# Kernel optimization log

Hardware: AMD Instinct MI355X
Metric: run time of the kernel (lower is better)

Reference implementation:

```python
import jax, jax.numpy as jnp
import numpy as np

N = 100000
E = 1600000
NIN = 128
NOUT = 128


def setup_inputs() -> dict:
    key = jax.random.key(0)
    k1, k2, k3, k4 = jax.random.split(key, 4)
    x = jax.random.normal(k1, (N, NIN), dtype=jnp.float32)
    edge_index = jax.random.randint(k2, (2, E), 0, N, dtype=jnp.int64)
    edge_attr = jnp.ones((E,), dtype=jnp.float32)  # unused by GCNConv
    # PyG Linear weight is [out, in]; glorot-ish init
    W = jax.random.normal(k3, (NOUT, NIN), dtype=jnp.float32) / np.sqrt(NIN)
    b = jnp.zeros((NOUT,), dtype=jnp.float32)
    return {"x": x, "edge_index": edge_index, "edge_attr": edge_attr, "W": W, "b": b}


def reference(x, edge_index, edge_attr, W, b):
    # PyG GCNConv: add self-loops, symmetric degree normalization,
    # linear transform, scatter-add aggregation at destination, + bias.
    n = x.shape[0]
    loops = jnp.arange(n, dtype=edge_index.dtype)
    src = jnp.concatenate([edge_index[0], loops])  # [E+N]
    dst = jnp.concatenate([edge_index[1], loops])  # [E+N]
    # degree over destination (col) including self-loops, edge weight = 1
    deg = jax.ops.segment_sum(jnp.ones_like(dst, dtype=x.dtype), dst, num_segments=n)
    dinv = jnp.where(deg > 0, jax.lax.rsqrt(deg), 0.0)
    norm = dinv[src] * dinv[dst]  # [E+N]
    h = x @ W.T  # [N, NOUT]
    msg = h[src] * norm[:, None]  # [E+N, NOUT]
    out = jax.ops.segment_sum(msg, dst, num_segments=n)  # [N, NOUT]
    return out + b
```

## Files before the change

### kernel.cpp

```cpp
#include <hip/hip_runtime.h>

#define TPB 256
#define NBLK 256
#define BSH 8

typedef __attribute__((ext_vector_type(4))) float f32x4;
typedef __attribute__((ext_vector_type(8))) short short8;

__device__ __forceinline__ unsigned short f2bf(float f) {
    unsigned u = __float_as_uint(f);
    u = (u + 0x7fffu + ((u >> 16) & 1u)) >> 16;
    return (unsigned short)u;
}
__device__ __forceinline__ float bflo(unsigned u) { return __uint_as_float(u << 16); }
__device__ __forceinline__ float bfhi(unsigned u) { return __uint_as_float(u & 0xffff0000u); }


__global__ __launch_bounds__(256) void k_bhist(const int* __restrict__ dst,
                                               int* __restrict__ btotal, int E, int NB) {
    __shared__ int sh[512];
    for (int i = threadIdx.x; i < NB; i += 256) sh[i] = 0;
    __syncthreads();
    int chunk = (E + NBLK - 1) / NBLK;
    int lo = blockIdx.x * chunk;
    int hi = min(E, lo + chunk);
    for (int e = lo + threadIdx.x; e < hi; e += 256)
        atomicAdd(&sh[dst[e] >> BSH], 1);
    __syncthreads();
    for (int i = threadIdx.x; i < NB; i += 256)
        if (sh[i]) atomicAdd(&btotal[i], sh[i]);
}


__global__ __launch_bounds__(512) void k_bscan(const int* __restrict__ btotal,
                                               int* __restrict__ bbase, int* __restrict__ bcur,
                                               int* __restrict__ offsets, int E, int NB, int N) {
    __shared__ int tmp[2][512];
    int t = threadIdx.x;
    int v = (t < NB) ? btotal[t] : 0;
    tmp[0][t] = v;
    __syncthreads();
    int sb = 0;
    for (int d = 1; d < 512; d <<= 1) {
        int val = tmp[sb][t];
        if (t >= d) val += tmp[sb][t - d];
        tmp[sb ^ 1][t] = val;
        sb ^= 1;
        __syncthreads();
    }
    int excl = tmp[sb][t] - v;
    if (t < NB) { bbase[t] = excl; bcur[t] = excl; }
    if (t == 0) { bbase[NB] = E; offsets[N] = E; }
}


__global__ __launch_bounds__(256) void k_bscatter(const int* __restrict__ src,
                                                  const int* __restrict__ dst,
                                                  int* __restrict__ bcur,
                                                  int2* __restrict__ pairs, int E, int NB) {
    __shared__ int sh[512];
    __shared__ int sbase[512];
    for (int i = threadIdx.x; i < NB; i += 256) sh[i] = 0;
    __syncthreads();
    int chunk = (E + NBLK - 1) / NBLK;
    int lo = blockIdx.x * chunk;
    int hi = min(E, lo + chunk);
    for (int e = lo + threadIdx.x; e < hi; e += 256)
        atomicAdd(&sh[dst[e] >> BSH], 1);
    __syncthreads();
    for (int i = threadIdx.x; i < NB; i += 256) {
        int c = sh[i];
        sbase[i] = c ? atomicAdd(&bcur[i], c) : 0;
    }
    __syncthreads();
    for (int i = threadIdx.x; i < NB; i += 256) sh[i] = sbase[i];
    __syncthreads();
    for (int e = lo + threadIdx.x; e < hi; e += 256) {
        int d = dst[e];
        int pos = atomicAdd(&sh[d >> BSH], 1);
        pairs[pos] = make_int2(d, src[e]);
    }
}


__global__ __launch_bounds__(256) void k_bcsr(const int2* __restrict__ pairs,
                                              const int* __restrict__ bbase,
                                              int* __restrict__ offsets,
                                              int* __restrict__ sorted_src,
                                              float* __restrict__ dinv, int N) {
    __shared__ int hist[256];
    __shared__ int tmp[2][256];
    __shared__ int scur[256];
    int b = blockIdx.x;
    int s0 = bbase[b], s1 = bbase[b + 1];
    int t = threadIdx.x;
    hist[t] = 0;
    __syncthreads();
    for (int e = s0 + t; e < s1; e += 256)
        atomicAdd(&hist[pairs[e].x & 255], 1);
    __syncthreads();
    int v = hist[t];
    tmp[0][t] = v;
    __syncthreads();
    int sb = 0;
    for (int d = 1; d < 256; d <<= 1) {
        int val = tmp[sb][t];
        if (t >= d) val += tmp[sb][t - d];
        tmp[sb ^ 1][t] = val;
        sb ^= 1;
        __syncthreads();
    }
    int gbase = s0 + (tmp[sb][t] - v);
    scur[t] = gbase;
    int d = (b << BSH) + t;
    if (d < N) { offsets[d] = gbase; dinv[d] = rsqrtf((float)v + 1.0f); }
    __syncthreads();
    for (int e = s0 + t; e < s1; e += 256) {
        int2 pr = pairs[e];
        int pos = atomicAdd(&scur[pr.x & 255], 1);
        sorted_src[pos] = pr.y;
    }
}


__global__ void k_castW(const float* __restrict__ W, unsigned short* __restrict__ Wt) {
    int i = blockIdx.x * TPB + threadIdx.x;
    if (i < 128 * 128) Wt[i] = f2bf(W[i]);
}


__global__ __launch_bounds__(256) void k_gemm(const float* __restrict__ x,
                                              const unsigned short* __restrict__ Wt,
                                              const float* __restrict__ dinv,
                                              unsigned short* __restrict__ g, int n) {
    __shared__ unsigned short wb[128][136];
    const int tid = threadIdx.x;

    for (int chunk = tid; chunk < 2048; chunk += 256) {
        int nrow = chunk >> 4, k8 = (chunk & 15) << 3;
        *(uint4*)&wb[nrow][k8] = ((const uint4*)Wt)[chunk];
    }
    __syncthreads();

    const int lane = tid & 63;
    const int wid  = tid >> 6;
    const int l15  = lane & 15;
    const int quad = lane >> 4;
    const int row  = blockIdx.x * 64 + wid * 16 + l15;
    const int rowc = (row < n) ? row : (n - 1);

    f32x4 acc[8];
    #pragma unroll
    for (int t = 0; t < 8; ++t) acc[t] = (f32x4){0.f, 0.f, 0.f, 0.f};

    #pragma unroll
    for (int ks = 0; ks < 4; ++ks) {
        const int kb = ks * 32 + quad * 8;
        float4 a0 = *(const float4*)(x + (long)rowc * 128 + kb);
        float4 a1 = *(const float4*)(x + (long)rowc * 128 + kb + 4);
        union { unsigned short u[8]; short8 v; } af;
        af.u[0] = f2bf(a0.x); af.u[1] = f2bf(a0.y); af.u[2] = f2bf(a0.z); af.u[3] = f2bf(a0.w);
        af.u[4] = f2bf(a1.x); af.u[5] = f2bf(a1.y); af.u[6] = f2bf(a1.z); af.u[7] = f2bf(a1.w);
        #pragma unroll
        for (int t = 0; t < 8; ++t) {
            short8 bf = *(const short8*)&wb[t * 16 + l15][kb];
            acc[t] = __builtin_amdgcn_mfma_f32_16x16x32_bf16(af.v, bf, acc[t], 0, 0, 0);
        }
    }

    int   orow[4];
    float dv[4];
    #pragma unroll
    for (int r = 0; r < 4; ++r) {
        orow[r] = blockIdx.x * 64 + wid * 16 + quad * 4 + r;
        dv[r]   = (orow[r] < n) ? dinv[orow[r]] : 0.f;
    }
    #pragma unroll
    for (int t = 0; t < 8; ++t) {
        int col = t * 16 + l15;
        #pragma unroll
        for (int r = 0; r < 4; ++r) {
            if (orow[r] < n)
                g[(long)orow[r] * 128 + col] = f2bf(acc[t][r] * dv[r]);
        }
    }
}


__global__ __launch_bounds__(256) void k_aggregate(const int* __restrict__ sorted_src,
                                                   const int* __restrict__ offsets,
                                                   const unsigned short* __restrict__ g,
                                                   const float* __restrict__ dinv,
                                                   const float* __restrict__ b,
                                                   float* __restrict__ out, int n) {
    int d = blockIdx.x * (TPB / 32) + (threadIdx.x >> 5);
    if (d >= n) return;
    int c = (threadIdx.x & 31) << 2;

    int s0 = offsets[d];
    int s1 = offsets[d + 1];

    float4 acc = make_float4(0.f, 0.f, 0.f, 0.f);
    auto addrow = [&](int r) {
        uint2 p = *(const uint2*)(g + (long)r * 128 + c);
        acc.x += bflo(p.x); acc.y += bfhi(p.x);
        acc.z += bflo(p.y); acc.w += bfhi(p.y);
    };

    addrow(d);
    int e = s0;
    for (; e + 8 <= s1; e += 8) {
        int a[8];
        #pragma unroll
        for (int j = 0; j < 8; ++j) a[j] = sorted_src[e + j];
        #pragma unroll
        for (int j = 0; j < 8; ++j) addrow(a[j]);
    }
    for (; e + 4 <= s1; e += 4) {
        int a[4];
        #pragma unroll
        for (int j = 0; j < 4; ++j) a[j] = sorted_src[e + j];
        #pragma unroll
        for (int j = 0; j < 4; ++j) addrow(a[j]);
    }
    for (; e < s1; ++e) addrow(sorted_src[e]);

    float s = dinv[d];
    float4 bb = *(const float4*)(b + c);
    float4 r = make_float4(acc.x * s + bb.x, acc.y * s + bb.y,
                           acc.z * s + bb.z, acc.w * s + bb.w);
    *(float4*)(out + (long)d * 128 + c) = r;
}


extern "C" void kernel_launch(void* const* d_in, const int* in_sizes, int n_in,
                              void* d_out, int out_size, void* d_ws, size_t ws_size,
                              hipStream_t stream) {
    const float* x  = (const float*)d_in[0];
    const int*   ei = (const int*)d_in[1];
    const float* W  = (const float*)d_in[3];
    const float* b  = (const float*)d_in[4];
    float* out = (float*)d_out;

    const int N = in_sizes[0] / 128;
    const int E = in_sizes[1] / 2;
    const int* src = ei;
    const int* dst = ei + E;
    const int NB = (N + 255) >> BSH;

    char* p = (char*)d_ws;
    auto carve = [&](size_t bytes) { char* q = p; p += (bytes + 255) & ~(size_t)255; return q; };
    int*            btotal     = (int*)           carve(512 * 4);
    int*            bbase      = (int*)           carve(513 * 4);
    int*            bcur       = (int*)           carve(512 * 4);
    int*            offsets    = (int*)           carve((size_t)(N + 1) * 4);
    float*          dinv       = (float*)         carve((size_t)N * 4);
    int2*           pairs      = (int2*)          carve((size_t)E * 8);
    int*            sorted_src = (int*)           carve((size_t)E * 4);
    unsigned short* Wt         = (unsigned short*)carve((size_t)128 * 128 * 2);
    unsigned short* g          = (unsigned short*)carve((size_t)N * 128 * 2);

    hipMemsetAsync(btotal, 0, 512 * 4, stream);

    k_bhist   <<<NBLK, TPB, 0, stream>>>(dst, btotal, E, NB);
    k_bscan   <<<1, 512, 0, stream>>>(btotal, bbase, bcur, offsets, E, NB, N);
    k_bscatter<<<NBLK, TPB, 0, stream>>>(src, dst, bcur, pairs, E, NB);
    k_bcsr    <<<NB, TPB, 0, stream>>>(pairs, bbase, offsets, sorted_src, dinv, N);

    k_castW<<<(128 * 128 + TPB - 1) / TPB, TPB, 0, stream>>>(W, Wt);
    k_gemm<<<(N + 63) / 64, TPB, 0, stream>>>(x, Wt, dinv, g, N);

    k_aggregate<<<(N + (TPB / 32) - 1) / (TPB / 32), TPB, 0, stream>>>(
        sorted_src, offsets, g, dinv, b, out, N);
}
```

Before: 254.6 us.

## Fuse bucket sort pipeline and W cast into one cooperative kernel

Replaces the memset, histogram, scan, scatter, CSR build and W-cast launches with a single cooperative kernel that uses grid-wide syncs between phases. Each block redoes the bucket scan locally instead of reading a separate bbase array, and the grid grows to 1024 blocks so each block handles a smaller edge chunk. The aim is to remove launch gaps and small serial kernels. The cost is grid.sync barriers, which need all 1024 blocks to be resident at once, and redundant scans in every block.

```diff
diff --git a/kernel.cpp b/kernel.cpp
--- a/kernel.cpp
+++ b/kernel.cpp
@@ -1,7 +1,10 @@
 #include <hip/hip_runtime.h>
+#include <hip/hip_cooperative_groups.h>
+
+namespace cg = cooperative_groups;
 
 #define TPB 256
-#define NBLK 256
+#define SORTBLKS 1024
 #define BSH 8
 
 typedef __attribute__((ext_vector_type(4))) float f32x4;
@@ -16,116 +19,111 @@
 __device__ __forceinline__ float bfhi(unsigned u) { return __uint_as_float(u & 0xffff0000u); }
 
 
-__global__ __launch_bounds__(256) void k_bhist(const int* __restrict__ dst,
-                                               int* __restrict__ btotal, int E, int NB) {
+__global__ __launch_bounds__(256, 4) void k_coopsort(
+    const int* __restrict__ src, const int* __restrict__ dst,
+    const float* __restrict__ W,
+    int* __restrict__ btotal, int* __restrict__ bcur,
+    int2* __restrict__ pairs, int* __restrict__ offsets,
+    int* __restrict__ sorted_src, float* __restrict__ dinv,
+    unsigned short* __restrict__ Wt, int E, int N, int NB)
+{
+    cg::grid_group grid = cg::this_grid();
     __shared__ int sh[512];
-    for (int i = threadIdx.x; i < NB; i += 256) sh[i] = 0;
-    __syncthreads();
-    int chunk = (E + NBLK - 1) / NBLK;
-    int lo = blockIdx.x * chunk;
-    int hi = min(E, lo + chunk);
-    for (int e = lo + threadIdx.x; e < hi; e += 256)
-        atomicAdd(&sh[dst[e] >> BSH], 1);
-    __syncthreads();
-    for (int i = threadIdx.x; i < NB; i += 256)
+    __shared__ int lbase[512];
+    __shared__ int stmp[2][512];
+    __shared__ int hist[256];
+    __shared__ int scur[256];
+
+    const int t = threadIdx.x;
+    const int nblocks = gridDim.x;
+    const long gtid = (long)blockIdx.x * 256 + t;
+    const long gsz = (long)nblocks * 256;
+    const int chunk = (E + nblocks - 1) / nblocks;
+    const int lo = blockIdx.x * chunk;
+    const int hi = min(E, lo + chunk);
+
+    for (long i = gtid; i < NB; i += gsz) btotal[i] = 0;
+    for (long i = gtid; i < 128 * 128; i += gsz) Wt[i] = f2bf(W[i]);
+    if (gtid == 0) offsets[N] = E;
+    grid.sync();
+
+    for (int i = t; i < NB; i += 256) sh[i] = 0;
+    __syncthreads();
+    for (int e = lo + t; e < hi; e += 256) atomicAdd(&sh[dst[e] >> BSH], 1);
+    __syncthreads();
+    for (int i = t; i < NB; i += 256)
         if (sh[i]) atomicAdd(&btotal[i], sh[i]);
-}
-
-
-__global__ __launch_bounds__(512) void k_bscan(const int* __restrict__ btotal,
-                                               int* __restrict__ bbase, int* __restrict__ bcur,
-                                               int* __restrict__ offsets, int E, int NB, int N) {
-    __shared__ int tmp[2][512];
-    int t = threadIdx.x;
-    int v = (t < NB) ? btotal[t] : 0;
-    tmp[0][t] = v;
-    __syncthreads();
-    int sb = 0;
-    for (int d = 1; d < 512; d <<= 1) {
-        int val = tmp[sb][t];
-        if (t >= d) val += tmp[sb][t - d];
-        tmp[sb ^ 1][t] = val;
-        sb ^= 1;
-        __syncthreads();
-    }
-    int excl = tmp[sb][t] - v;
-    if (t < NB) { bbase[t] = excl; bcur[t] = excl; }
-    if (t == 0) { bbase[NB] = E; offsets[N] = E; }
-}
-
-
-__global__ __launch_bounds__(256) void k_bscatter(const int* __restrict__ src,
-                                                  const int* __restrict__ dst,
-                                                  int* __restrict__ bcur,
-                                                  int2* __restrict__ pairs, int E, int NB) {
-    __shared__ int sh[512];
-    __shared__ int sbase[512];
-    for (int i = threadIdx.x; i < NB; i += 256) sh[i] = 0;
-    __syncthreads();
-    int chunk = (E + NBLK - 1) / NBLK;
-    int lo = blockIdx.x * chunk;
-    int hi = min(E, lo + chunk);
-    for (int e = lo + threadIdx.x; e < hi; e += 256)
-        atomicAdd(&sh[dst[e] >> BSH], 1);
-    __syncthreads();
-    for (int i = threadIdx.x; i < NB; i += 256) {
+    grid.sync();
+
+    {
+        int v0 = (t < NB) ? btotal[t] : 0;
+        int v1 = (t + 256 < NB) ? btotal[t + 256] : 0;
+        stmp[0][t] = v0; stmp[0][t + 256] = v1;
+        __syncthreads();
+        int sb = 0;
+        for (int d = 1; d < 512; d <<= 1) {
+            int a = stmp[sb][t]       + ((t       >= d) ? stmp[sb][t - d]       : 0);
+            int bv = stmp[sb][t + 256] + ((t + 256 >= d) ? stmp[sb][t + 256 - d] : 0);
+            stmp[sb ^ 1][t] = a; stmp[sb ^ 1][t + 256] = bv;
+            sb ^= 1;
+            __syncthreads();
+        }
+        lbase[t]       = stmp[sb][t]       - v0;
+        lbase[t + 256] = stmp[sb][t + 256] - v1;
+        __syncthreads();
+        if (blockIdx.x == 0) {
+            if (t < NB) bcur[t] = lbase[t];
+            if (t + 256 < NB) bcur[t + 256] = lbase[t + 256];
+        }
+    }
+    grid.sync();
+
+    for (int i = t; i < NB; i += 256) sh[i] = 0;
+    __syncthreads();
+    for (int e = lo + t; e < hi; e += 256) atomicAdd(&sh[dst[e] >> BSH], 1);
+    __syncthreads();
+    for (int i = t; i < NB; i += 256) {
         int c = sh[i];
-        sbase[i] = c ? atomicAdd(&bcur[i], c) : 0;
-    }
-    __syncthreads();
-    for (int i = threadIdx.x; i < NB; i += 256) sh[i] = sbase[i];
-    __syncthreads();
-    for (int e = lo + threadIdx.x; e < hi; e += 256) {
+        sh[i] = c ? atomicAdd(&bcur[i], c) : 0;
+    }
+    __syncthreads();
+    for (int e = lo + t; e < hi; e += 256) {
         int d = dst[e];
         int pos = atomicAdd(&sh[d >> BSH], 1);
         pairs[pos] = make_int2(d, src[e]);
     }
-}
-
-
-__global__ __launch_bounds__(256) void k_bcsr(const int2* __restrict__ pairs,
-                                              const int* __restrict__ bbase,
-                                              int* __restrict__ offsets,
-                                              int* __restrict__ sorted_src,
-                                              float* __restrict__ dinv, int N) {
-    __shared__ int hist[256];
-    __shared__ int tmp[2][256];
-    __shared__ int scur[256];
-    int b = blockIdx.x;
-    int s0 = bbase[b], s1 = bbase[b + 1];
-    int t = threadIdx.x;
-    hist[t] = 0;
-    __syncthreads();
-    for (int e = s0 + t; e < s1; e += 256)
-        atomicAdd(&hist[pairs[e].x & 255], 1);
-    __syncthreads();
-    int v = hist[t];
-    tmp[0][t] = v;
-    __syncthreads();
-    int sb = 0;
-    for (int d = 1; d < 256; d <<= 1) {
-        int val = tmp[sb][t];
-        if (t >= d) val += tmp[sb][t - d];
-        tmp[sb ^ 1][t] = val;
-        sb ^= 1;
-        __syncthreads();
-    }
-    int gbase = s0 + (tmp[sb][t] - v);
-    scur[t] = gbase;
-    int d = (b << BSH) + t;
-    if (d < N) { offsets[d] = gbase; dinv[d] = rsqrtf((float)v + 1.0f); }
-    __syncthreads();
-    for (int e = s0 + t; e < s1; e += 256) {
-        int2 pr = pairs[e];
-        int pos = atomicAdd(&scur[pr.x & 255], 1);
-        sorted_src[pos] = pr.y;
-    }
-}
-
-
-__global__ void k_castW(const float* __restrict__ W, unsigned short* __restrict__ Wt) {
-    int i = blockIdx.x * TPB + threadIdx.x;
-    if (i < 128 * 128) Wt[i] = f2bf(W[i]);
+    grid.sync();
+
+    for (int b = blockIdx.x; b < NB; b += nblocks) {
+        int s0 = lbase[b];
+        int s1 = (b + 1 < 512) ? lbase[b + 1] : E;
+        hist[t] = 0;
+        __syncthreads();
+        for (int e = s0 + t; e < s1; e += 256)
+            atomicAdd(&hist[pairs[e].x & 255], 1);
+        __syncthreads();
+        int v = hist[t];
+        stmp[0][t] = v;
+        __syncthreads();
+        int sb = 0;
+        for (int d = 1; d < 256; d <<= 1) {
+            int val = stmp[sb][t] + ((t >= d) ? stmp[sb][t - d] : 0);
+            stmp[sb ^ 1][t] = val;
+            sb ^= 1;
+            __syncthreads();
+        }
+        int gbase = s0 + stmp[sb][t] - v;
+        scur[t] = gbase;
+        int d = (b << BSH) + t;
+        if (d < N) { offsets[d] = gbase; dinv[d] = rsqrtf((float)v + 1.0f); }
+        __syncthreads();
+        for (int e = s0 + t; e < s1; e += 256) {
+            int2 pr = pairs[e];
+            int pos = atomicAdd(&scur[pr.x & 255], 1);
+            sorted_src[pos] = pr.y;
+        }
+        __syncthreads();
+    }
 }
 
 
@@ -251,7 +249,6 @@
     char* p = (char*)d_ws;
     auto carve = [&](size_t bytes) { char* q = p; p += (bytes + 255) & ~(size_t)255; return q; };
     int*            btotal     = (int*)           carve(512 * 4);
-    int*            bbase      = (int*)           carve(513 * 4);
     int*            bcur       = (int*)           carve(512 * 4);
     int*            offsets    = (int*)           carve((size_t)(N + 1) * 4);
     float*          dinv       = (float*)         carve((size_t)N * 4);
@@ -260,14 +257,14 @@
     unsigned short* Wt         = (unsigned short*)carve((size_t)128 * 128 * 2);
     unsigned short* g          = (unsigned short*)carve((size_t)N * 128 * 2);
 
-    hipMemsetAsync(btotal, 0, 512 * 4, stream);
-
-    k_bhist   <<<NBLK, TPB, 0, stream>>>(dst, btotal, E, NB);
-    k_bscan   <<<1, 512, 0, stream>>>(btotal, bbase, bcur, offsets, E, NB, N);
-    k_bscatter<<<NBLK, TPB, 0, stream>>>(src, dst, bcur, pairs, E, NB);
-    k_bcsr    <<<NB, TPB, 0, stream>>>(pairs, bbase, offsets, sorted_src, dinv, N);
-
-    k_castW<<<(128 * 128 + TPB - 1) / TPB, TPB, 0, stream>>>(W, Wt);
+    int Ev = E, Nv = N, NBv = NB;
+    void* args[] = {(void*)&src, (void*)&dst, (void*)&W,
+                    (void*)&btotal, (void*)&bcur, (void*)&pairs,
+                    (void*)&offsets, (void*)&sorted_src, (void*)&dinv,
+                    (void*)&Wt, (void*)&Ev, (void*)&Nv, (void*)&NBv};
+    hipLaunchCooperativeKernel((const void*)k_coopsort, dim3(SORTBLKS), dim3(TPB),
+                               args, 0, stream);
+
     k_gemm<<<(N + 63) / 64, TPB, 0, stream>>>(x, Wt, dinv, g, N);
 
     k_aggregate<<<(N + (TPB / 32) - 1) / (TPB / 32), TPB, 0, stream>>>(
```

New measurement: 664.2 us. +160.9%, slower.
